# Kernel tuning notes

Hardware: AMD Instinct MI355X
Metric: run time of the kernel (lower is better)

The kernel has to match this reference:

```python
import jax, jax.numpy as jnp
import numpy as np

D, H, K, L, NB = 128, 8, 16, 16, 2
N, E, MN, ME = 100_000, 800_000, 1_000, 8_000
VOCAB, BT, VP = 50_000, 256, 15
_SQD, _SQK = float(np.sqrt(D)), float(np.sqrt(K))


def _segment_softmax(score, seg, num):
    m = jax.ops.segment_max(score, seg, num_segments=num)
    e = jnp.exp(score - m[seg])
    z = jax.ops.segment_sum(e, seg, num_segments=num)
    return e / (z[seg] + 1e-9)


def _meta_learner(feat, u, W2, W1):
    # latent-attention factorization: feat [n,D] -> 2d param [n,H,K], 1d param [n,H]
    w = jax.nn.softmax((feat @ u.T) / _SQD, axis=-1)  # [n,L]
    return jnp.einsum('nl,lhk->nhk', w, W2), w @ W1


def _conv(feat, src, dst, p2n, p1n, p2e, p1e, Wq, Wk, Wv, Wo):
    # HeteroAttnConv: multi-head attention message passing modulated by
    # per-node (p2n,p1n) and per-edge (p2e,p1e) meta parameters.
    n = feat.shape[0]
    q = (feat @ Wq).reshape(n, H, K) * p2n
    kf = (feat @ Wk).reshape(n, H, K)
    v = (feat @ Wv).reshape(n, H, K)
    ke = kf[src] * p2e                                   # [e,H,K]
    score = (q[dst] * ke).sum(-1) / _SQK + p1e + p1n[dst]  # [e,H]
    attn = _segment_softmax(score, dst, n)
    agg = jax.ops.segment_sum(attn[..., None] * v[src], dst, num_segments=n).reshape(n, D)
    return jax.nn.relu(agg @ Wo), ke.reshape(-1, D)


def _forward(emb, u, W2lat, W1lat, Wq_m, Wk_m, Wv_m, Wo_m, Wq, Wk, Wv, Wo,
             node_vals, meta_node_vals, src, dst, meta_src, meta_dst,
             meta_node_id, meta_edge_id, target_idx,
             static_vals, static_src, static_dst):
    # _init_meta_param: static param-name graph, copy_u/sum then meta_learner
    fs = emb[static_vals]
    agg = jax.ops.segment_sum(fs[static_src], static_dst, num_segments=VP)
    p2s, p1s = _meta_learner(agg, u, W2lat, W1lat)
    base_tw, base_n1, base_n2 = p1s[0], p1s[3], p2s[6]   # target_weight, node 1d, node 2d
    base_e1, base_e2 = p1s[9], p2s[12]                   # edge 1d, edge 2d

    meta_feat = emb[meta_node_vals]
    feat = emb[node_vals]
    # _asign_param_to_graph(meta_graph): broadcast base buffers only
    mp2n = jnp.broadcast_to(base_n2, (MN, H, K))
    mp1n = jnp.broadcast_to(base_n1, (MN, H))
    mp2e = jnp.broadcast_to(base_e2, (ME, H, K))
    mp1e = jnp.broadcast_to(base_e1, (ME, H))

    out = jnp.zeros((BT, 1), feat.dtype)
    for b in range(NB):
        pre_meta, pre = meta_feat, feat
        meta_feat, meta_edge_feat = _conv(meta_feat, meta_src, meta_dst,
                                          mp2n, mp1n, mp2e, mp1e,
                                          Wq_m[b], Wk_m[b], Wv_m[b], Wo_m[b])
        # _asign_param_to_graph(graph, meta_node_feat, meta_edge_feat):
        # base repeat + indexed add of meta_learner outputs
        p2mn, p1mn = _meta_learner(meta_feat, u, W2lat, W1lat)
        p2me, p1me = _meta_learner(meta_edge_feat, u, W2lat, W1lat)
        p2n = base_n2[None] + p2mn[meta_node_id]
        p1n = base_n1[None] + p1mn[meta_node_id]
        tw = base_tw[None] + p1mn[meta_node_id]
        p2e = base_e2[None] + p2me[meta_edge_id]
        p1e = base_e1[None] + p1me[meta_edge_id]
        feat, _ = _conv(feat, src, dst, p2n, p1n, p2e, p1e,
                        Wq[b], Wk[b], Wv[b], Wo[b])
        # block residual
        meta_feat = meta_feat + pre_meta
        feat = feat + pre
        # Target: per-target-node weighted readout with target_weight param
        logit = jnp.einsum('th,thk->t', tw[target_idx],
                           feat[target_idx].reshape(BT, H, K))
        out = out + logit[:, None]
    return out / NB


def setup_inputs() -> dict:
    key = jax.random.key(0)
    ks = jax.random.split(key, 24)
    s = 0.05
    inp = {}
    inp['emb'] = jax.random.normal(ks[0], (VOCAB, D), jnp.float32) * s
    inp['u'] = jax.random.normal(ks[1], (L, D), jnp.float32) * s
    inp['W2lat'] = jax.random.normal(ks[2], (L, H, K), jnp.float32) * s
    inp['W1lat'] = jax.random.normal(ks[3], (L, H), jnp.float32) * s
    for i, nm in enumerate(['Wq_m', 'Wk_m', 'Wv_m', 'Wo_m', 'Wq', 'Wk', 'Wv', 'Wo']):
        inp[nm] = jax.random.normal(ks[4 + i], (NB, D, D), jnp.float32) / np.sqrt(D)
    inp['node_vals'] = jax.random.randint(ks[12], (N,), 0, VOCAB)
    inp['meta_node_vals'] = jax.random.randint(ks[13], (MN,), 0, VOCAB)
    inp['src'] = jax.random.randint(ks[14], (E,), 0, N)
    inp['dst'] = jax.random.randint(ks[15], (E,), 0, N)
    inp['meta_src'] = jax.random.randint(ks[16], (ME,), 0, MN)
    inp['meta_dst'] = jax.random.randint(ks[17], (ME,), 0, MN)
    inp['meta_node_id'] = jax.random.randint(ks[18], (N,), 0, MN)
    inp['meta_edge_id'] = jax.random.randint(ks[19], (E,), 0, ME)
    inp['target_idx'] = jax.random.randint(ks[20], (BT,), 0, N)
    # static param-name graph: 5 names x (1 name node + 2 token nodes), tokens->name
    name_pos = np.arange(5) * 3
    inp['static_vals'] = jax.random.randint(ks[21], (VP,), 0, VOCAB)
    inp['static_src'] = jnp.asarray(np.stack([name_pos + 1, name_pos + 2], 1).reshape(-1), jnp.int32)
    inp['static_dst'] = jnp.asarray(np.repeat(name_pos, 2), jnp.int32)
    return inp


def reference(emb, u, W2lat, W1lat, Wq_m, Wk_m, Wv_m, Wo_m, Wq, Wk, Wv, Wo,
              node_vals, meta_node_vals, src, dst, meta_src, meta_dst,
              meta_node_id, meta_edge_id, target_idx,
              static_vals, static_src, static_dst):
    return _forward(emb, u, W2lat, W1lat, Wq_m, Wk_m, Wv_m, Wo_m, Wq, Wk, Wv, Wo,
                    node_vals, meta_node_vals, src, dst, meta_src, meta_dst,
                    meta_node_id, meta_edge_id, target_idx,
                    static_vals, static_src, static_dst)
```

## Files before the change

### kernel.cpp

```cpp
#include <hip/hip_runtime.h>
#include <hip/hip_bf16.h>
#include <hip/hip_fp8.h>

#define DD   128
#define HH   8

typedef short bf16x8 __attribute__((ext_vector_type(8)));
typedef float f32x4  __attribute__((ext_vector_type(4)));
typedef float f32x2  __attribute__((ext_vector_type(2)));

__device__ __forceinline__ float b2f(unsigned short v){
  union { unsigned int u; float f; } x; x.u = ((unsigned int)v) << 16; return x.f;
}
__device__ __forceinline__ unsigned short f2b(float f){
  __hip_bfloat16 h = __float2bfloat16(f);
  return *(unsigned short*)&h;
}
__device__ __forceinline__ unsigned char f2f8(float x){
  __hip_fp8_e4m3 h(x);
  return h.__x;
}
__device__ __forceinline__ float f82f(unsigned char b){
  __hip_fp8_e4m3 h; h.__x = b;
  return (float)h;
// ... 11 lines not shown
  o[2]=f82f((w>>16)&0xff); o[3]=f82f((w>>24)&0xff);
}
struct __align__(8) us4 { unsigned short x,y,z,w; };
struct __align__(16) us8 { unsigned short s[8]; };

__device__ __forceinline__ float gld(const void* p, size_t i, bool f32){
  if (f32) return ((const float*)p)[i];
  return b2f(((const unsigned short*)p)[i]);
}

__device__ __forceinline__ void gll16(const void* g, void* l){
  __builtin_amdgcn_global_load_lds(
      (const __attribute__((address_space(1))) unsigned int*)g,
      (__attribute__((address_space(3))) unsigned int*)l, 16, 0, 0);
}

struct WPtrs { const void* p[8]; };
__global__ __launch_bounds__(256) void w_repack16(
    WPtrs W, unsigned short* __restrict__ stage, int NBt,
    const int* __restrict__ dflag)
{
  const bool wf32 = (*dflag) != 0;
  int idx = blockIdx.x >> 6;
  int ti = idx / NBt, bi = idx - ti*NBt;
  size_t bo = (size_t)bi*DD*DD;
  int i = (blockIdx.x & 63)*256 + threadIdx.x;
  int k = i >> 7, n = i & 127;
  float x;
  if (wf32) x = ((const float*)W.p[ti])[bo + i];
  else      x = b2f(((const unsigned short*)W.p[ti])[bo + i]);
  stage[(size_t)idx*DD*DD + n*DD + k] = f2b(x);
}

enum { EPI_STORE=0, EPI_SCALE_CONST=1, EPI_SCALE_GATHER=2, EPI_RELU=3,
       EPI_RELU_RES=4, EPI_RELU_RES2=5 };

#define CPAD 132


template<int EPI, bool INB, bool OUTB>
__global__ __launch_bounds__(256) void gemm128m(
    const void* __restrict__ Av, const unsigned short* __restrict__ Bt,
    void* __restrict__ Cv, int M,
    const unsigned short* __restrict__ Rb,
    const float* __restrict__ Rf, float* __restrict__ C2)
{
  __shared__ __align__(16) unsigned short Asb[64*128];
  __shared__ __align__(16) unsigned short Btb[16896];
  const int tid = threadIdx.x;
  const int wave = tid >> 6, lane = tid & 63;
  const int row0 = blockIdx.x * 64;

  if (INB){
    const char* Ab = (const char*)Av;
    int n4 = lane >> 4, c = lane & 15;
#pragma unroll
    for (int op=0; op<4; op++){
      int rA = wave*16 + op*4;
      int n = rA + n4;
      int gr = row0 + n; if (gr >= M) gr = M - 1;
      gll16(Ab + (size_t)gr*256 + ((size_t)((c ^ (n & 7)) << 4)), &Asb[rA*128]);
    }
  } else {
    const float* Af = (const float*)Av;
    int r = tid >> 2, cb = (tid & 3) * 32, rx = (r & 7) << 3;
    int gr = row0 + r;
#pragma unroll
// ... 44 lines not shown
  }
  __syncthreads();

  {
    int r = tid >> 2, cb = (tid & 3) * 32;
    int gr = row0 + r;
    if (gr < M){
#pragma unroll
      for (int j=0;j<8;j++){
        int c = cb + j*4;
        float4 o = *(float4*)&Cls[r*CPAD + c];
        if (EPI == EPI_RELU_RES){
          us4 rb = *(const us4*)(Rb + (size_t)gr*DD + c);
          o.x=fmaxf(o.x,0.f)+b2f(rb.x); o.y=fmaxf(o.y,0.f)+b2f(rb.y);
          o.z=fmaxf(o.z,0.f)+b2f(rb.z); o.w=fmaxf(o.w,0.f)+b2f(rb.w);
        } else if (EPI == EPI_RELU_RES2){
          o.x=fmaxf(o.x,0.f); o.y=fmaxf(o.y,0.f); o.z=fmaxf(o.z,0.f); o.w=fmaxf(o.w,0.f);
          float4 rf = *(const float4*)(Rf + (size_t)gr*DD + c);
          *(float4*)(C2 + (size_t)gr*DD + c) =
              make_float4(o.x+rf.x, o.y+rf.y, o.z+rf.z, o.w+rf.w);
        }
        if (OUTB){
          us4 ob; ob.x=f2b(o.x); ob.y=f2b(o.y); ob.z=f2b(o.z); ob.w=f2b(o.w);
          *(us4*)((unsigned short*)Cv + (size_t)gr*DD + c) = ob;
        } else {
          *(float4*)((float*)Cv + (size_t)gr*DD + c) = o;
        }
      }
    }
  }
}

template<int EPIQ, bool INB, bool FP8KV>
__global__ __launch_bounds__(256) void gemm_qkv(
    const void* __restrict__ Av,
    const unsigned short* __restrict__ Btq, const unsigned short* __restrict__ Btk,
    const unsigned short* __restrict__ Btv,
    void* __restrict__ Cq, void* __restrict__ Ck, int stK,
    void* __restrict__ Cvo, int stV, int M,
    const float* __restrict__ svec, const float* __restrict__ P2,
    const int* __restrict__ gidx)
{
  __shared__ __align__(16) unsigned short Asb[64*128];
  __shared__ __align__(16) unsigned short Btb[16896];
  const int tid = threadIdx.x;
  const int wave = tid >> 6, lane = tid & 63;
  const int row0 = blockIdx.x * 64;

  if (INB){
    const char* Ab = (const char*)Av;
    int n4 = lane >> 4, c = lane & 15;
#pragma unroll
    for (int op=0; op<4; op++){
      int rA = wave*16 + op*4;
      int n = rA + n4;
      int gr = row0 + n; if (gr >= M) gr = M - 1;
      gll16(Ab + (size_t)gr*256 + ((size_t)((c ^ (n & 7)) << 4)), &Asb[rA*128]);
    }
  } else {
    const float* Af = (const float*)Av;
    int r = tid >> 2, cb = (tid & 3) * 32, rx = (r & 7) << 3;
    int gr = row0 + r;
#pragma unroll
    for (int j=0;j<8;j++){
      int cc = cb + j*4;
      float4 val = make_float4(0.f,0.f,0.f,0.f);
      if (gr < M) val = *(const float4*)(Af + (size_t)gr*DD + cc);
      us4 o; o.x=f2b(val.x); o.y=f2b(val.y); o.z=f2b(val.z); o.w=f2b(val.w);
      *(us4*)&Asb[r*128 + (cc ^ rx)] = o;
    }
  }

  const unsigned short* Bts[3] = {Btq, Btk, Btv};
  void* Cs[3] = {Cq, Ck, Cvo};
  const int sts[3] = {DD, stK, stV};
  const int am = (lane & 15), kq = (lane >> 4) * 8, axr = (am & 7) << 3;

  for (int ph=0; ph<3; ph++){
    {
      const unsigned short* Bt = Bts[ph];
// ... 10 lines not shown
    f32x4 acc[8];
#pragma unroll
    for (int t=0;t<8;t++) acc[t] = (f32x4){0.f,0.f,0.f,0.f};
#pragma unroll
    for (int k0=0;k0<128;k0+=32){
      int xo = (k0 + kq) ^ axr;
      bf16x8 a = *(bf16x8*)&Asb[(wave*16 + am)*128 + xo];
#pragma unroll
      for (int t=0;t<8;t++){
        bf16x8 b = *(bf16x8*)&Btb[(t*16 + am)*128 + xo];
        acc[t] = __builtin_amdgcn_mfma_f32_16x16x32_bf16(a, b, acc[t], 0,0,0);
      }
    }
    __syncthreads();
    float* Cls = (float*)Btb;
    {
      int rr = wave*16 + (lane>>4)*4;
      int cc = lane & 15;
#pragma unroll
      for (int t=0;t<8;t++)
#pragma unroll
        for (int r=0;r<4;r++)
          Cls[(rr + r)*CPAD + t*16 + cc] = acc[t][r];
    }
    __syncthreads();
    {
      int r = tid >> 2, cb = (tid & 3) * 32;
      int gr = row0 + r;
      if (gr < M){
#pragma unroll
        for (int j=0;j<8;j++){
          int c = cb + j*4;
          float4 o = *(float4*)&Cls[r*CPAD + c];
          if (ph == 0){
            if (EPIQ == EPI_SCALE_GATHER){
              int g = gidx[gr];
              const float* p = P2 + (size_t)g*DD + c;
              o.x*=(svec[c+0]+p[0]); o.y*=(svec[c+1]+p[1]);
              o.z*=(svec[c+2]+p[2]); o.w*=(svec[c+3]+p[3]);
            } else {
              o.x*=svec[c+0]; o.y*=svec[c+1]; o.z*=svec[c+2]; o.w*=svec[c+3];
            }
          }
          if (FP8KV && ph > 0){
            unsigned char* Cb = (unsigned char*)Cs[ph];
            uchar4 ob;
            ob.x=f2f8(o.x*8.f); ob.y=f2f8(o.y*8.f);
            ob.z=f2f8(o.z*8.f); ob.w=f2f8(o.w*8.f);
            *(uchar4*)(Cb + (size_t)gr*256 + c) = ob;
          } else {
            us4 ob; ob.x=f2b(o.x); ob.y=f2b(o.y); ob.z=f2b(o.z); ob.w=f2b(o.w);
            *(us4*)((unsigned short*)Cs[ph] + (size_t)gr*sts[ph] + c) = ob;
          }
        }
      }
    }
    __syncthreads();
  }
}

__global__ __launch_bounds__(256) void k_static(
    const void* __restrict__ emb, const int* __restrict__ svals,
    const int* __restrict__ ssrc, const int* __restrict__ sdst,
    const void* __restrict__ u, const void* __restrict__ W2,
    const void* __restrict__ W1, float* __restrict__ base, int nsrc,
    int* __restrict__ dflag)
{
  __shared__ float sagg[15][128];
  __shared__ float ssc[15][16];
  __shared__ float sww[15][16];
  __shared__ int swf;
  const int t = threadIdx.x;
  if (t < 64){
    float m = 0.f;
    for (int i=t; i<128; i+=64){
      float x = fabsf(b2f(((const unsigned short*)emb)[i]));
      if (x < 1e30f) m = fmaxf(m, x);
    }
#pragma unroll
    for (int s=1;s<64;s<<=1) m = fmaxf(m, __shfl_xor(m, s, 64));
    if (t==0){ int f = (m > 1e4f) ? 1 : 0; *dflag = f; swf = f; }
  }
  for (int i=t;i<15*128;i+=256) ((float*)sagg)[i]=0.f;
  __syncthreads();
  const bool wf32 = (swf != 0);
  if (t < 128){
    for (int i=0;i<nsrc;i++){
      int row = sdst[i]; int vr = svals[ssrc[i]];
      sagg[row][t] += gld(emb, (size_t)vr*DD + t, wf32);
    }
// ... 192 lines not shown
  if (d >= NM) return;
  int lane = threadIdx.x & 63;
  const float* be2 = base+152; const float* be1 = base+16; const float* bn1 = base+8;
  size_t dq = (size_t)d*DD;
  float q0 = b2f(qm[dq+lane]), q1 = b2f(qm[dq+64+lane]);
  float w0 = be2[lane], w1 = be2[64+lane];
  int h0 = lane>>4, h1 = h0+4;
  float bias0 = be1[h0] + bn1[h0];
  float bias1 = be1[h1] + bn1[h1];
  float z0=0.f, z1=0.f, a0=0.f, a1=0.f;
  int i0 = rowptr[d], i1 = rowptr[d+1];
  for (int i=i0; i<i1; i++){
    int s = esrc[i], e = eorig[i];
    size_t so=(size_t)s*DD, eo=(size_t)e*DD;
    float ke0 = b2f(kfm[so+lane])    * w0;
    float ke1 = b2f(kfm[so+64+lane]) * w1;
    mef[eo+lane]=f2b(ke0); mef[eo+64+lane]=f2b(ke1);
    float p0 = q0*ke0, p1 = q1*ke1;
#pragma unroll
    for (int m=1;m<16;m<<=1){ p0 += __shfl_xor(p0,m,64); p1 += __shfl_xor(p1,m,64); }
    float e0 = __expf(p0*0.25f + bias0);
    float e1 = __expf(p1*0.25f + bias1);
    z0 += e0; z1 += e1;
    a0 += e0*b2f(vm[so+lane]);
    a1 += e1*b2f(vm[so+64+lane]);
  }
  float inv0 = 1.f/(z0 + 1e-9f);
  float inv1 = 1.f/(z1 + 1e-9f);
  agg[dq+lane]    = a0*inv0;
  agg[dq+64+lane] = a1*inv1;
}

__global__ __launch_bounds__(128) void learner2(
    const float* __restrict__ Xa, const unsigned short* __restrict__ Xb, int Ma,
    const void* __restrict__ u, const void* __restrict__ W2,
    const void* __restrict__ W1,
    float* __restrict__ p2a, float* __restrict__ p1a,
    unsigned short* __restrict__ w2me, unsigned short* __restrict__ p1b,
    const float* __restrict__ base, const int* __restrict__ dflag)
{
  __shared__ float sX[128];
  __shared__ float st[16];
  __shared__ float sw[16];
  const bool wf32 = (*dflag) != 0;
  const int blk = blockIdx.x, t = threadIdx.x;
  const bool isB = (blk >= Ma);
  const int m = isB ? (blk - Ma) : blk;
  if (isB) sX[t] = b2f(Xb[(size_t)m*DD + t]);
  else     sX[t] = Xa[(size_t)m*DD + t];
  __syncthreads();
  int l = t>>3, j = t&7;
  float part = 0.f;
  for (int d=j*16; d<j*16+16; d++) part += sX[d]*gld(u, l*128+d, wf32);
  part += __shfl_xor(part,1,64); part += __shfl_xor(part,2,64); part += __shfl_xor(part,4,64);
  if (j==0) st[l] = part * 0.08838834764831845f;
  __syncthreads();
  float mx=-1e30f;
  for (int i=0;i<16;i++) mx = fmaxf(mx, st[i]);
  float ssum=0.f;
  for (int i=0;i<16;i++) ssum += __expf(st[i]-mx);
  float inv = 1.f/ssum;
  if (t<16) sw[t] = __expf(st[t]-mx)*inv;
  __syncthreads();
  float a=0.f;
  for (int i=0;i<16;i++) a += sw[i]*gld(W2, i*128+t, wf32);
  if (isB) w2me[(size_t)m*DD+t] = f2b(base[152+t] + a);
  else     p2a[(size_t)m*DD+t] = a;
  if (t<8){
    float bb=0.f;
    for (int i=0;i<16;i++) bb += sw[i]*gld(W1, i*8+t, wf32);
    if (isB) p1b[(size_t)m*HH+t] = f2b(bb);
    else     p1a[(size_t)m*HH+t] = bb;
  }
}

__global__ __launch_bounds__(256) void edge_fused(
    const int* __restrict__ rowptr, const int* __restrict__ epack,
    const int* __restrict__ mnid,
    const unsigned short* __restrict__ q, const unsigned char* __restrict__ kv8,
    const unsigned short* __restrict__ w2me, const unsigned short* __restrict__ p1me,
    const float* __restrict__ p1mn, const float* __restrict__ base,
    unsigned short* __restrict__ aggb, int N)
{
  int wv = blockIdx.x*4 + (threadIdx.x>>6);
  int lane = threadIdx.x & 63;
  int grp = lane >> 4, l16 = lane & 15;
  int d = wv*4 + grp;
  if (d >= N) return;
  int c8 = l16 * 8;
  int h = l16 >> 1;

  int i0 = rowptr[d], i1 = rowptr[d+1];
  float bias = base[16+h] + base[8+h] + p1mn[(size_t)mnid[d]*HH + h];
  size_t dq = (size_t)d*DD;
  float qv[8];
  {
    uint4 qraw = *(const uint4*)(q + dq + c8);
    const unsigned short* qh = (const unsigned short*)&qraw;
#pragma unroll
    for (int j=0;j<8;j++) qv[j] = b2f(qh[j])*0.03125f;
  }

  float zh = 0.f;
  float a[8];
#pragma unroll
  for (int j=0;j<8;j++) a[j] = 0.f;

  int i = i0;
  for (; i + 1 < i1; i += 2){
    unsigned int v0p = (unsigned int)epack[i];
    unsigned int v1p = (unsigned int)epack[i+1];
    int s0 = v0p & 0x1FFFF, me0 = v0p >> 17;
    int s1 = v1p & 0x1FFFF, me1 = v1p >> 17;
    size_t kvo0 = (size_t)s0*256, mo0 = (size_t)me0*DD;
    size_t kvo1 = (size_t)s1*256, mo1 = (size_t)me1*DD;
    uint2 kraw0 = *(const uint2*)(kv8 + kvo0 + c8);
    uint2 vraw0 = *(const uint2*)(kv8 + kvo0 + 128 + c8);
    uint4 wraw0 = *(const uint4*)(w2me + mo0 + c8);
    float pm0 = b2f(p1me[(size_t)me0*HH + h]);
    uint2 kraw1 = *(const uint2*)(kv8 + kvo1 + c8);
    uint2 vraw1 = *(const uint2*)(kv8 + kvo1 + 128 + c8);
    uint4 wraw1 = *(const uint4*)(w2me + mo1 + c8);
    float pm1 = b2f(p1me[(size_t)me1*HH + h]);
    float k0f[8], v0f[8], k1f[8], v1f[8];
    cvt4(kraw0.x, k0f); cvt4(kraw0.y, k0f+4);
    cvt4(vraw0.x, v0f); cvt4(vraw0.y, v0f+4);
    cvt4(kraw1.x, k1f); cvt4(kraw1.y, k1f+4);
    cvt4(vraw1.x, v1f); cvt4(vraw1.y, v1f+4);
    const unsigned short* wh0 = (const unsigned short*)&wraw0;
    const unsigned short* wh1 = (const unsigned short*)&wraw1;
    float pA = 0.f, pB = 0.f;
#pragma unroll
    for (int j=0;j<8;j++){
      pA += qv[j]*(k0f[j]*b2f(wh0[j]));
      pB += qv[j]*(k1f[j]*b2f(wh1[j]));
    }
    pA += __shfl_xor(pA, 1, 64);
    pB += __shfl_xor(pB, 1, 64);
    float ex0 = __expf(pA + bias + pm0);
    float ex1 = __expf(pB + bias + pm1);
    zh += ex0 + ex1;
#pragma unroll
    for (int j=0;j<8;j++) a[j] += ex0*v0f[j] + ex1*v1f[j];
  }
  if (i < i1){
    unsigned int vp = (unsigned int)epack[i];
    int s = vp & 0x1FFFF, me = vp >> 17;
    size_t kvo = (size_t)s*256, mo = (size_t)me*DD;
    uint2 kraw = *(const uint2*)(kv8 + kvo + c8);
    uint2 vraw = *(const uint2*)(kv8 + kvo + 128 + c8);
    uint4 wraw = *(const uint4*)(w2me + mo + c8);
    float pm = b2f(p1me[(size_t)me*HH + h]);
    float kf[8], vf[8];
    cvt4(kraw.x, kf); cvt4(kraw.y, kf+4);
    cvt4(vraw.x, vf); cvt4(vraw.y, vf+4);
    const unsigned short* wh = (const unsigned short*)&wraw;
    float p = 0.f;
#pragma unroll
    for (int j=0;j<8;j++) p += qv[j]*(kf[j]*b2f(wh[j]));
    p += __shfl_xor(p, 1, 64);
    float ex = __expf(p + bias + pm);
    zh += ex;
#pragma unroll
    for (int j=0;j<8;j++) a[j] += ex*vf[j];
  }

  float inv = 0.125f / (zh + 1e-9f);
  us8 o;
#pragma unroll
  for (int j=0;j<8;j++) o.s[j] = f2b(a[j]*inv);
  *(us8*)(aggb + dq + c8) = o;
}

__global__ __launch_bounds__(256) void readout(
    const int* __restrict__ tgt, const int* __restrict__ mnid,
    const unsigned short* __restrict__ featb, const float* __restrict__ p1mn,
    const float* __restrict__ base, float* __restrict__ acc,
    void* __restrict__ out, int last, float invNB, int BT,
    const int* __restrict__ dflag)
{
  int t = blockIdx.x*256 + threadIdx.x;
  int ti = t >> 4, l16 = t & 15;
  if (ti >= BT) return;
  int idx = tgt[ti]; int mn = mnid[idx];
  int h = l16 >> 1;
  float tw = base[h] + p1mn[(size_t)mn*HH + h];
  uint4 raw = *(const uint4*)(featb + (size_t)idx*DD + l16*8);
  const unsigned short* hw = (const unsigned short*)&raw;
  float s = 0.f;
#pragma unroll
  for (int j=0;j<8;j++) s += b2f(hw[j]);
  float part = tw * s;
  part += __shfl_xor(part, 1, 64);
  part += __shfl_xor(part, 2, 64);
  part += __shfl_xor(part, 4, 64);
  part += __shfl_xor(part, 8, 64);
  if (l16 == 0){
    if (!last) acc[ti] = part;
    else {
      float r = (acc[ti] + part) * invNB;
      if ((*dflag) != 0) ((float*)out)[ti] = r;
      else ((__hip_bfloat16*)out)[ti] = __float2bfloat16(r);
    }
  }
// ... 73 lines not shown

  k_static<<<1,256,0,stream>>>(emb, static_vals, static_src, static_dst,
                               u, W2lat, W1lat, base, NSRC, dflag);
  gather_rows2<<<((N+MN)*16+255)/256,256,0,stream>>>(emb, node_vals, feat, N,
      meta_node_vals, meta_feat, MN, dflag);

  const int nbE  = (E+255)/256, nbME = (ME+255)/256;
  const int nb3B = (N+255)/256, nb3M = (MN+255)/256;
  zeroi<<<(N+MN+255)/256,256,0,stream>>>(degAll, N+MN);
  k_hist2<<<nbE+nbME,256,0,stream>>>(dst, meta_dst, deg, deg_m, E, ME, nbE);
  k_scan1b<<<nb_scan+nb_scan_m,256,0,stream>>>(deg, rowptr, bsum, N, nb_scan,
      deg_m, rowptr_m, bsum_m, MN);
  k_scan3b<<<nb3B+nb3M,256,0,stream>>>(rowptr, bsum, cursor, N, nb3B, nb_scan,
      rowptr_m, bsum_m, cursor_m, MN, nb_scan_m);
  k_scatter2<<<nbE+nbME,256,0,stream>>>(dst, src, meta_edge_id, cursor,
      epack, E, nbE, meta_dst, meta_src, cursor_m, esrc_m, eorig_m, ME);

  w_repack16<<<8*NB*64,256,0,stream>>>(wptrs, wstage, NB, dflag);

  const int gm = (MN+63)/64;
  const int gN = (N+63)/64;
  const float invNB = 1.0f/(float)NB;

  for (int b=0;b<NB;b++){
    const unsigned short* wq_m = wstage + (size_t)(0*NB+b)*DD*DD;
    const unsigned short* wk_m = wstage + (size_t)(1*NB+b)*DD*DD;
    const unsigned short* wv_m = wstage + (size_t)(2*NB+b)*DD*DD;
    const unsigned short* wo_m = wstage + (size_t)(3*NB+b)*DD*DD;
    const unsigned short* wqb  = wstage + (size_t)(4*NB+b)*DD*DD;
    const unsigned short* wkb  = wstage + (size_t)(5*NB+b)*DD*DD;
    const unsigned short* wvb  = wstage + (size_t)(6*NB+b)*DD*DD;
    const unsigned short* wob  = wstage + (size_t)(7*NB+b)*DD*DD;

    gemm_qkv<EPI_SCALE_CONST,false,false><<<gm,256,0,stream>>>(meta_feat,
        wq_m, wk_m, wv_m, q_m, kf_m, DD, v_m, DD, MN, base_n2, nullptr, nullptr);
    edge_meta_csr<<<(MN+3)/4,256,0,stream>>>(rowptr_m, esrc_m, eorig_m,
        q_m, kf_m, v_m, base, mef, agg_m, MN);
    gemm128m<EPI_RELU_RES2,false,false><<<gm,256,0,stream>>>(agg_m, wo_m,
        meta_out, MN, nullptr, meta_feat, meta_feat);
    learner2<<<MN+ME,128,0,stream>>>(meta_out, mef, MN, u, W2lat, W1lat,
        p2mn, p1mn, w2me, p1me, base, dflag);

    gemm_qkv<EPI_SCALE_GATHER,true,true><<<gN,256,0,stream>>>(feat, wqb, wkb, wvb,
        q, kv8, 0, kv8 + 128, 0, N, base_n2, p2mn, meta_node_id);
    edge_fused<<<(N+15)/16,256,0,stream>>>(rowptr, epack,
        meta_node_id, q, kv8, w2me, p1me, p1mn, base, aggb, N);
    gemm128m<EPI_RELU_RES,true,true><<<gN,256,0,stream>>>(aggb, wob, feat, N,
        feat, nullptr, nullptr);

    readout<<<(BT*16+255)/256,256,0,stream>>>(target_idx, meta_node_id, feat, p1mn,
        base, acc, d_out, (b==NB-1) ? 1 : 0, invNB, BT, dflag);
  }
}
```

Baseline: 647.9 us.

## Merge big and meta QKV GEMMs, defer node q-scaling into edge kernel

The big-graph QKV projection no longer depends on the meta learner output. The per-node p2 scale is now applied to q inside the edge attention kernel, so the big and meta QKV GEMMs run as one launch before the meta stage. The edge kernel switches from 16 lanes per destination to 8 lanes per destination (one per head), which drops the cross-lane shuffle. learner2 caches u/W2/W1 in registers and handles four rows per block. The trade-offs are higher register pressure in the edge kernel and a q stored in bf16 before it is scaled.

```diff
diff --git a/kernel.cpp b/kernel.cpp
--- a/kernel.cpp
+++ b/kernel.cpp
@@ -67,7 +67,7 @@
   stage[(size_t)idx*DD*DD + n*DD + k] = f2b(x);
 }
 
-enum { EPI_STORE=0, EPI_SCALE_CONST=1, EPI_SCALE_GATHER=2, EPI_RELU=3,
+enum { EPI_STORE=0, EPI_SCALE_CONST=1, EPI_RELU=3,
        EPI_RELU_RES=4, EPI_RELU_RES2=5 };
 
 #define CPAD 132
@@ -178,20 +178,18 @@
 }
 
 template<int EPIQ, bool INB, bool FP8KV>
-__global__ __launch_bounds__(256) void gemm_qkv(
+__device__ __forceinline__ void qkv_body(
+    unsigned short* Asb, unsigned short* Btb, int blk,
     const void* __restrict__ Av,
     const unsigned short* __restrict__ Btq, const unsigned short* __restrict__ Btk,
     const unsigned short* __restrict__ Btv,
     void* __restrict__ Cq, void* __restrict__ Ck, int stK,
     void* __restrict__ Cvo, int stV, int M,
-    const float* __restrict__ svec, const float* __restrict__ P2,
-    const int* __restrict__ gidx)
+    const float* __restrict__ svec)
 {
-  __shared__ __align__(16) unsigned short Asb[64*128];
-  __shared__ __align__(16) unsigned short Btb[16896];
   const int tid = threadIdx.x;
   const int wave = tid >> 6, lane = tid & 63;
-  const int row0 = blockIdx.x * 64;
+  const int row0 = blk * 64;
 
   if (INB){
     const char* Ab = (const char*)Av;
@@ -268,15 +266,8 @@
         for (int j=0;j<8;j++){
           int c = cb + j*4;
           float4 o = *(float4*)&Cls[r*CPAD + c];
-          if (ph == 0){
-            if (EPIQ == EPI_SCALE_GATHER){
-              int g = gidx[gr];
-              const float* p = P2 + (size_t)g*DD + c;
-              o.x*=(svec[c+0]+p[0]); o.y*=(svec[c+1]+p[1]);
-              o.z*=(svec[c+2]+p[2]); o.w*=(svec[c+3]+p[3]);
-            } else {
-              o.x*=svec[c+0]; o.y*=svec[c+1]; o.z*=svec[c+2]; o.w*=svec[c+3];
-            }
+          if (ph == 0 && EPIQ == EPI_SCALE_CONST){
+            o.x*=svec[c+0]; o.y*=svec[c+1]; o.z*=svec[c+2]; o.w*=svec[c+3];
           }
           if (FP8KV && ph > 0){
             unsigned char* Cb = (unsigned char*)Cs[ph];
@@ -292,6 +283,28 @@
       }
     }
     __syncthreads();
+  }
+}
+
+__global__ __launch_bounds__(256) void gemm_qkv2(
+    const unsigned short* __restrict__ featB, const float* __restrict__ featM,
+    const unsigned short* __restrict__ wqb, const unsigned short* __restrict__ wkb,
+    const unsigned short* __restrict__ wvb,
+    const unsigned short* __restrict__ wqm, const unsigned short* __restrict__ wkm,
+    const unsigned short* __restrict__ wvm,
+    unsigned short* __restrict__ qB, unsigned char* __restrict__ kv8,
+    unsigned short* __restrict__ qM, unsigned short* __restrict__ kfM,
+    unsigned short* __restrict__ vM,
+    int Nbig, int Nmeta, int gN, const float* __restrict__ svec)
+{
+  __shared__ __align__(16) unsigned short Asb[64*128];
+  __shared__ __align__(16) unsigned short Btb[16896];
+  if (blockIdx.x < gN){
+    qkv_body<EPI_STORE,true,true>(Asb, Btb, blockIdx.x, featB,
+        wqb, wkb, wvb, qB, kv8, 0, kv8 + 128, 0, Nbig, svec);
+  } else {
+    qkv_body<EPI_SCALE_CONST,false,false>(Asb, Btb, blockIdx.x - gN, featM,
+        wqm, wkm, wvm, qM, kfM, DD, vM, DD, Nmeta, svec);
   }
 }
 
@@ -550,7 +563,8 @@
 }
 
 __global__ __launch_bounds__(128) void learner2(
-    const float* __restrict__ Xa, const unsigned short* __restrict__ Xb, int Ma,
+    const float* __restrict__ Xa, const unsigned short* __restrict__ Xb,
+    int Ma, int Mtot,
     const void* __restrict__ u, const void* __restrict__ W2,
     const void* __restrict__ W1,
     float* __restrict__ p2a, float* __restrict__ p1a,
@@ -561,34 +575,51 @@
   __shared__ float st[16];
   __shared__ float sw[16];
   const bool wf32 = (*dflag) != 0;
-  const int blk = blockIdx.x, t = threadIdx.x;
-  const bool isB = (blk >= Ma);
-  const int m = isB ? (blk - Ma) : blk;
-  if (isB) sX[t] = b2f(Xb[(size_t)m*DD + t]);
-  else     sX[t] = Xa[(size_t)m*DD + t];
-  __syncthreads();
-  int l = t>>3, j = t&7;
-  float part = 0.f;
-  for (int d=j*16; d<j*16+16; d++) part += sX[d]*gld(u, l*128+d, wf32);
-  part += __shfl_xor(part,1,64); part += __shfl_xor(part,2,64); part += __shfl_xor(part,4,64);
-  if (j==0) st[l] = part * 0.08838834764831845f;
-  __syncthreads();
-  float mx=-1e30f;
-  for (int i=0;i<16;i++) mx = fmaxf(mx, st[i]);
-  float ssum=0.f;
-  for (int i=0;i<16;i++) ssum += __expf(st[i]-mx);
-  float inv = 1.f/ssum;
-  if (t<16) sw[t] = __expf(st[t]-mx)*inv;
-  __syncthreads();
-  float a=0.f;
-  for (int i=0;i<16;i++) a += sw[i]*gld(W2, i*128+t, wf32);
-  if (isB) w2me[(size_t)m*DD+t] = f2b(base[152+t] + a);
-  else     p2a[(size_t)m*DD+t] = a;
-  if (t<8){
-    float bb=0.f;
-    for (int i=0;i<16;i++) bb += sw[i]*gld(W1, i*8+t, wf32);
-    if (isB) p1b[(size_t)m*HH+t] = f2b(bb);
-    else     p1a[(size_t)m*HH+t] = bb;
+  const int t = threadIdx.x;
+  const int l = t>>3, j = t&7;
+  float uc[16], w2c[16], w1c[16];
+#pragma unroll
+  for (int m=0;m<16;m++) uc[m] = gld(u, (size_t)l*128 + j*16 + m, wf32);
+#pragma unroll
+  for (int i=0;i<16;i++) w2c[i] = gld(W2, (size_t)i*128 + t, wf32);
+  if (t < 8){
+#pragma unroll
+    for (int i=0;i<16;i++) w1c[i] = gld(W1, (size_t)i*8 + t, wf32);
+  }
+  for (int rr=0; rr<4; rr++){
+    int row = blockIdx.x*4 + rr;
+    if (row >= Mtot) break;
+    const bool isB = (row >= Ma);
+    const int m = isB ? (row - Ma) : row;
+    if (isB) sX[t] = b2f(Xb[(size_t)m*DD + t]);
+    else     sX[t] = Xa[(size_t)m*DD + t];
+    __syncthreads();
+    float part = 0.f;
+#pragma unroll
+    for (int mm=0;mm<16;mm++) part += sX[j*16+mm]*uc[mm];
+    part += __shfl_xor(part,1,64); part += __shfl_xor(part,2,64); part += __shfl_xor(part,4,64);
+    if (j==0) st[l] = part * 0.08838834764831845f;
+    __syncthreads();
+    float mx=-1e30f;
+    for (int i=0;i<16;i++) mx = fmaxf(mx, st[i]);
+    float ssum=0.f;
+    for (int i=0;i<16;i++) ssum += __expf(st[i]-mx);
+    float inv = 1.f/ssum;
+    if (t<16) sw[t] = __expf(st[t]-mx)*inv;
+    __syncthreads();
+    float a=0.f;
+#pragma unroll
+    for (int i=0;i<16;i++) a += sw[i]*w2c[i];
+    if (isB) w2me[(size_t)m*DD+t] = f2b(base[152+t] + a);
+    else     p2a[(size_t)m*DD+t] = a;
+    if (t<8){
+      float bb=0.f;
+#pragma unroll
+      for (int i=0;i<16;i++) bb += sw[i]*w1c[i];
+      if (isB) p1b[(size_t)m*HH+t] = f2b(bb);
+      else     p1a[(size_t)m*HH+t] = bb;
+    }
+    __syncthreads();
   }
 }
 
@@ -597,32 +628,40 @@
     const int* __restrict__ mnid,
     const unsigned short* __restrict__ q, const unsigned char* __restrict__ kv8,
     const unsigned short* __restrict__ w2me, const unsigned short* __restrict__ p1me,
-    const float* __restrict__ p1mn, const float* __restrict__ base,
+    const float* __restrict__ p1mn, const float* __restrict__ p2mn,
+    const float* __restrict__ base,
     unsigned short* __restrict__ aggb, int N)
 {
-  int wv = blockIdx.x*4 + (threadIdx.x>>6);
-  int lane = threadIdx.x & 63;
-  int grp = lane >> 4, l16 = lane & 15;
-  int d = wv*4 + grp;
+  const int tid = threadIdx.x;
+  const int lane = tid & 63;
+  const int l8 = lane & 7;
+  const int d = blockIdx.x*32 + (tid>>6)*8 + (lane>>3);
   if (d >= N) return;
-  int c8 = l16 * 8;
-  int h = l16 >> 1;
-
-  int i0 = rowptr[d], i1 = rowptr[d+1];
-  float bias = base[16+h] + base[8+h] + p1mn[(size_t)mnid[d]*HH + h];
-  size_t dq = (size_t)d*DD;
-  float qv[8];
+  const int h = l8;
+  const int c16 = l8*16;
+  const int i0 = rowptr[d], i1 = rowptr[d+1];
+  const int mn = mnid[d];
+  const float bias = base[16+h] + base[8+h] + p1mn[(size_t)mn*HH + h];
+  const size_t dq = (size_t)d*DD;
+
+  float qv[16];
   {
-    uint4 qraw = *(const uint4*)(q + dq + c8);
-    const unsigned short* qh = (const unsigned short*)&qraw;
-#pragma unroll
-    for (int j=0;j<8;j++) qv[j] = b2f(qh[j])*0.03125f;
+    uint4 qr0 = *(const uint4*)(q + dq + c16);
+    uint4 qr1 = *(const uint4*)(q + dq + c16 + 8);
+    const unsigned short* qh0 = (const unsigned short*)&qr0;
+    const unsigned short* qh1 = (const unsigned short*)&qr1;
+    const float* p2 = p2mn + (size_t)mn*DD + c16;
+    const float* sv = base + 24 + c16;
+#pragma unroll
+    for (int j=0;j<8;j++) qv[j]   = b2f(qh0[j]) * (sv[j]   + p2[j])   * 0.03125f;
+#pragma unroll
+    for (int j=0;j<8;j++) qv[8+j] = b2f(qh1[j]) * (sv[8+j] + p2[8+j]) * 0.03125f;
   }
 
   float zh = 0.f;
-  float a[8];
-#pragma unroll
-  for (int j=0;j<8;j++) a[j] = 0.f;
+  float a[16];
+#pragma unroll
+  for (int j=0;j<16;j++) a[j] = 0.f;
 
   int i = i0;
   for (; i + 1 < i1; i += 2){
@@ -630,64 +669,79 @@
     unsigned int v1p = (unsigned int)epack[i+1];
     int s0 = v0p & 0x1FFFF, me0 = v0p >> 17;
     int s1 = v1p & 0x1FFFF, me1 = v1p >> 17;
-    size_t kvo0 = (size_t)s0*256, mo0 = (size_t)me0*DD;
-    size_t kvo1 = (size_t)s1*256, mo1 = (size_t)me1*DD;
-    uint2 kraw0 = *(const uint2*)(kv8 + kvo0 + c8);
-    uint2 vraw0 = *(const uint2*)(kv8 + kvo0 + 128 + c8);
-    uint4 wraw0 = *(const uint4*)(w2me + mo0 + c8);
+    const unsigned char* kv0 = kv8 + (size_t)s0*256 + c16;
+    const unsigned char* kv1 = kv8 + (size_t)s1*256 + c16;
+    const unsigned short* w0 = w2me + (size_t)me0*DD + c16;
+    const unsigned short* w1 = w2me + (size_t)me1*DD + c16;
+    uint4 kraw0 = *(const uint4*)kv0;
+    uint4 vraw0 = *(const uint4*)(kv0 + 128);
+    us8 w0a = *(const us8*)w0;
+    us8 w0b = *(const us8*)(w0 + 8);
     float pm0 = b2f(p1me[(size_t)me0*HH + h]);
-    uint2 kraw1 = *(const uint2*)(kv8 + kvo1 + c8);
-    uint2 vraw1 = *(const uint2*)(kv8 + kvo1 + 128 + c8);
-    uint4 wraw1 = *(const uint4*)(w2me + mo1 + c8);
+    uint4 kraw1 = *(const uint4*)kv1;
+    uint4 vraw1 = *(const uint4*)(kv1 + 128);
+    us8 w1a = *(const us8*)w1;
+    us8 w1b = *(const us8*)(w1 + 8);
     float pm1 = b2f(p1me[(size_t)me1*HH + h]);
-    float k0f[8], v0f[8], k1f[8], v1f[8];
-    cvt4(kraw0.x, k0f); cvt4(kraw0.y, k0f+4);
-    cvt4(vraw0.x, v0f); cvt4(vraw0.y, v0f+4);
-    cvt4(kraw1.x, k1f); cvt4(kraw1.y, k1f+4);
-    cvt4(vraw1.x, v1f); cvt4(vraw1.y, v1f+4);
-    const unsigned short* wh0 = (const unsigned short*)&wraw0;
-    const unsigned short* wh1 = (const unsigned short*)&wraw1;
+
+    float k0f[16], k1f[16];
+    cvt4(kraw0.x,k0f);   cvt4(kraw0.y,k0f+4);
+    cvt4(kraw0.z,k0f+8); cvt4(kraw0.w,k0f+12);
+    cvt4(kraw1.x,k1f);   cvt4(kraw1.y,k1f+4);
+    cvt4(kraw1.z,k1f+8); cvt4(kraw1.w,k1f+12);
     float pA = 0.f, pB = 0.f;
 #pragma unroll
     for (int j=0;j<8;j++){
-      pA += qv[j]*(k0f[j]*b2f(wh0[j]));
-      pB += qv[j]*(k1f[j]*b2f(wh1[j]));
-    }
-    pA += __shfl_xor(pA, 1, 64);
-    pB += __shfl_xor(pB, 1, 64);
+      pA += qv[j]  *(k0f[j]  *b2f(w0a.s[j]));
+      pA += qv[8+j]*(k0f[8+j]*b2f(w0b.s[j]));
+      pB += qv[j]  *(k1f[j]  *b2f(w1a.s[j]));
+      pB += qv[8+j]*(k1f[8+j]*b2f(w1b.s[j]));
+    }
     float ex0 = __expf(pA + bias + pm0);
     float ex1 = __expf(pB + bias + pm1);
     zh += ex0 + ex1;
-#pragma unroll
-    for (int j=0;j<8;j++) a[j] += ex0*v0f[j] + ex1*v1f[j];
+    float v0f[16], v1f[16];
+    cvt4(vraw0.x,v0f);   cvt4(vraw0.y,v0f+4);
+    cvt4(vraw0.z,v0f+8); cvt4(vraw0.w,v0f+12);
+    cvt4(vraw1.x,v1f);   cvt4(vraw1.y,v1f+4);
+    cvt4(vraw1.z,v1f+8); cvt4(vraw1.w,v1f+12);
+#pragma unroll
+    for (int j=0;j<16;j++) a[j] += ex0*v0f[j] + ex1*v1f[j];
   }
   if (i < i1){
     unsigned int vp = (unsigned int)epack[i];
     int s = vp & 0x1FFFF, me = vp >> 17;
-    size_t kvo = (size_t)s*256, mo = (size_t)me*DD;
-    uint2 kraw = *(const uint2*)(kv8 + kvo + c8);
-    uint2 vraw = *(const uint2*)(kv8 + kvo + 128 + c8);
-    uint4 wraw = *(const uint4*)(w2me + mo + c8);
+    const unsigned char* kv0 = kv8 + (size_t)s*256 + c16;
+    const unsigned short* w0 = w2me + (size_t)me*DD + c16;
+    uint4 kraw = *(const uint4*)kv0;
+    uint4 vraw = *(const uint4*)(kv0 + 128);
+    us8 wa = *(const us8*)w0;
+    us8 wb = *(const us8*)(w0 + 8);
     float pm = b2f(p1me[(size_t)me*HH + h]);
-    float kf[8], vf[8];
-    cvt4(kraw.x, kf); cvt4(kraw.y, kf+4);
-    cvt4(vraw.x, vf); cvt4(vraw.y, vf+4);
-    const unsigned short* wh = (const unsigned short*)&wraw;
+    float kf[16];
+    cvt4(kraw.x,kf);   cvt4(kraw.y,kf+4);
+    cvt4(kraw.z,kf+8); cvt4(kraw.w,kf+12);
     float p = 0.f;
 #pragma unroll
-    for (int j=0;j<8;j++) p += qv[j]*(kf[j]*b2f(wh[j]));
-    p += __shfl_xor(p, 1, 64);
+    for (int j=0;j<8;j++){
+      p += qv[j]  *(kf[j]  *b2f(wa.s[j]));
+      p += qv[8+j]*(kf[8+j]*b2f(wb.s[j]));
+    }
     float ex = __expf(p + bias + pm);
     zh += ex;
-#pragma unroll
-    for (int j=0;j<8;j++) a[j] += ex*vf[j];
+    float vf[16];
+    cvt4(vraw.x,vf);   cvt4(vraw.y,vf+4);
+    cvt4(vraw.z,vf+8); cvt4(vraw.w,vf+12);
+#pragma unroll
+    for (int j=0;j<16;j++) a[j] += ex*vf[j];
   }
 
   float inv = 0.125f / (zh + 1e-9f);
-  us8 o;
-#pragma unroll
-  for (int j=0;j<8;j++) o.s[j] = f2b(a[j]*inv);
-  *(us8*)(aggb + dq + c8) = o;
+  us8 o0, o1;
+#pragma unroll
+  for (int j=0;j<8;j++){ o0.s[j] = f2b(a[j]*inv); o1.s[j] = f2b(a[8+j]*inv); }
+  *(us8*)(aggb + dq + c16)     = o0;
+  *(us8*)(aggb + dq + c16 + 8) = o1;
 }
 
 __global__ __launch_bounds__(256) void readout(
@@ -827,19 +881,19 @@
     const unsigned short* wvb  = wstage + (size_t)(6*NB+b)*DD*DD;
     const unsigned short* wob  = wstage + (size_t)(7*NB+b)*DD*DD;
 
-    gemm_qkv<EPI_SCALE_CONST,false,false><<<gm,256,0,stream>>>(meta_feat,
-        wq_m, wk_m, wv_m, q_m, kf_m, DD, v_m, DD, MN, base_n2, nullptr, nullptr);
+    gemm_qkv2<<<gN+gm,256,0,stream>>>(feat, meta_feat,
+        wqb, wkb, wvb, wq_m, wk_m, wv_m,
+        q, kv8, q_m, kf_m, v_m, N, MN, gN, base_n2);
+
     edge_meta_csr<<<(MN+3)/4,256,0,stream>>>(rowptr_m, esrc_m, eorig_m,
         q_m, kf_m, v_m, base, mef, agg_m, MN);
     gemm128m<EPI_RELU_RES2,false,false><<<gm,256,0,stream>>>(agg_m, wo_m,
         meta_out, MN, nullptr, meta_feat, meta_feat);
-    learner2<<<MN+ME,128,0,stream>>>(meta_out, mef, MN, u, W2lat, W1lat,
-        p2mn, p1mn, w2me, p1me, base, dflag);
-
-    gemm_qkv<EPI_SCALE_GATHER,true,true><<<gN,256,0,stream>>>(feat, wqb, wkb, wvb,
-        q, kv8, 0, kv8 + 128, 0, N, base_n2, p2mn, meta_node_id);
-    edge_fused<<<(N+15)/16,256,0,stream>>>(rowptr, epack,
-        meta_node_id, q, kv8, w2me, p1me, p1mn, base, aggb, N);
+    learner2<<<(MN+ME+3)/4,128,0,stream>>>(meta_out, mef, MN, MN+ME,
+        u, W2lat, W1lat, p2mn, p1mn, w2me, p1me, base, dflag);
+
+    edge_fused<<<(N+31)/32,256,0,stream>>>(rowptr, epack,
+        meta_node_id, q, kv8, w2me, p1me, p1mn, p2mn, base, aggb, N);
     gemm128m<EPI_RELU_RES,true,true><<<gN,256,0,stream>>>(aggb, wob, feat, N,
         feat, nullptr, nullptr);
 
```

Measured after the change: 573.9 us. 11.4% less time.

## Merge big and meta QKV GEMMs, defer q scaling to edge kernel, batch learner rows

Applied to the files above, without the earlier changes.

The big-graph QKV GEMM no longer needs the per-meta-node q scale, so that scale moves into the edge attention kernel. This lets it run in the same launch as the meta-graph QKV GEMM, ahead of the meta conv chain, which cuts one launch and removes a dependency. learner2 now handles four rows per block and keeps u/W2/W1 in registers instead of reloading them for every row. The edge loop is unrolled by four to keep more gathers in flight, at the cost of extra register pressure and per-edge scale work in edge_fused.

```diff
diff --git a/kernel.cpp b/kernel.cpp
--- a/kernel.cpp
+++ b/kernel.cpp
@@ -67,7 +67,7 @@
   stage[(size_t)idx*DD*DD + n*DD + k] = f2b(x);
 }
 
-enum { EPI_STORE=0, EPI_SCALE_CONST=1, EPI_SCALE_GATHER=2, EPI_RELU=3,
+enum { EPI_STORE=0, EPI_SCALE_CONST=1, EPI_RELU=3,
        EPI_RELU_RES=4, EPI_RELU_RES2=5 };
 
 #define CPAD 132
@@ -178,20 +178,18 @@
 }
 
 template<int EPIQ, bool INB, bool FP8KV>
-__global__ __launch_bounds__(256) void gemm_qkv(
+__device__ __forceinline__ void qkv_body(
+    unsigned short* Asb, unsigned short* Btb, int blk,
     const void* __restrict__ Av,
     const unsigned short* __restrict__ Btq, const unsigned short* __restrict__ Btk,
     const unsigned short* __restrict__ Btv,
     void* __restrict__ Cq, void* __restrict__ Ck, int stK,
     void* __restrict__ Cvo, int stV, int M,
-    const float* __restrict__ svec, const float* __restrict__ P2,
-    const int* __restrict__ gidx)
+    const float* __restrict__ svec)
 {
-  __shared__ __align__(16) unsigned short Asb[64*128];
-  __shared__ __align__(16) unsigned short Btb[16896];
   const int tid = threadIdx.x;
   const int wave = tid >> 6, lane = tid & 63;
-  const int row0 = blockIdx.x * 64;
+  const int row0 = blk * 64;
 
   if (INB){
     const char* Ab = (const char*)Av;
@@ -268,15 +266,8 @@
         for (int j=0;j<8;j++){
           int c = cb + j*4;
           float4 o = *(float4*)&Cls[r*CPAD + c];
-          if (ph == 0){
-            if (EPIQ == EPI_SCALE_GATHER){
-              int g = gidx[gr];
-              const float* p = P2 + (size_t)g*DD + c;
-              o.x*=(svec[c+0]+p[0]); o.y*=(svec[c+1]+p[1]);
-              o.z*=(svec[c+2]+p[2]); o.w*=(svec[c+3]+p[3]);
-            } else {
-              o.x*=svec[c+0]; o.y*=svec[c+1]; o.z*=svec[c+2]; o.w*=svec[c+3];
-            }
+          if (ph == 0 && EPIQ == EPI_SCALE_CONST){
+            o.x*=svec[c+0]; o.y*=svec[c+1]; o.z*=svec[c+2]; o.w*=svec[c+3];
           }
           if (FP8KV && ph > 0){
             unsigned char* Cb = (unsigned char*)Cs[ph];
@@ -292,6 +283,28 @@
       }
     }
     __syncthreads();
+  }
+}
+
+__global__ __launch_bounds__(256) void gemm_qkv2(
+    const unsigned short* __restrict__ featB, const float* __restrict__ featM,
+    const unsigned short* __restrict__ wqb, const unsigned short* __restrict__ wkb,
+    const unsigned short* __restrict__ wvb,
+    const unsigned short* __restrict__ wqm, const unsigned short* __restrict__ wkm,
+    const unsigned short* __restrict__ wvm,
+    unsigned short* __restrict__ qB, unsigned char* __restrict__ kv8,
+    unsigned short* __restrict__ qM, unsigned short* __restrict__ kfM,
+    unsigned short* __restrict__ vM,
+    int Nbig, int Nmeta, int gN, const float* __restrict__ svec)
+{
+  __shared__ __align__(16) unsigned short Asb[64*128];
+  __shared__ __align__(16) unsigned short Btb[16896];
+  if (blockIdx.x < gN){
+    qkv_body<EPI_STORE,true,true>(Asb, Btb, blockIdx.x, featB,
+        wqb, wkb, wvb, qB, kv8, 0, kv8 + 128, 0, Nbig, svec);
+  } else {
+    qkv_body<EPI_SCALE_CONST,false,false>(Asb, Btb, blockIdx.x - gN, featM,
+        wqm, wkm, wvm, qM, kfM, DD, vM, DD, Nmeta, svec);
   }
 }
 
@@ -550,7 +563,8 @@
 }
 
 __global__ __launch_bounds__(128) void learner2(
-    const float* __restrict__ Xa, const unsigned short* __restrict__ Xb, int Ma,
+    const float* __restrict__ Xa, const unsigned short* __restrict__ Xb,
+    int Ma, int Mtot,
     const void* __restrict__ u, const void* __restrict__ W2,
     const void* __restrict__ W1,
     float* __restrict__ p2a, float* __restrict__ p1a,
@@ -561,34 +575,51 @@
   __shared__ float st[16];
   __shared__ float sw[16];
   const bool wf32 = (*dflag) != 0;
-  const int blk = blockIdx.x, t = threadIdx.x;
-  const bool isB = (blk >= Ma);
-  const int m = isB ? (blk - Ma) : blk;
-  if (isB) sX[t] = b2f(Xb[(size_t)m*DD + t]);
-  else     sX[t] = Xa[(size_t)m*DD + t];
-  __syncthreads();
-  int l = t>>3, j = t&7;
-  float part = 0.f;
-  for (int d=j*16; d<j*16+16; d++) part += sX[d]*gld(u, l*128+d, wf32);
-  part += __shfl_xor(part,1,64); part += __shfl_xor(part,2,64); part += __shfl_xor(part,4,64);
-  if (j==0) st[l] = part * 0.08838834764831845f;
-  __syncthreads();
-  float mx=-1e30f;
-  for (int i=0;i<16;i++) mx = fmaxf(mx, st[i]);
-  float ssum=0.f;
-  for (int i=0;i<16;i++) ssum += __expf(st[i]-mx);
-  float inv = 1.f/ssum;
-  if (t<16) sw[t] = __expf(st[t]-mx)*inv;
-  __syncthreads();
-  float a=0.f;
-  for (int i=0;i<16;i++) a += sw[i]*gld(W2, i*128+t, wf32);
-  if (isB) w2me[(size_t)m*DD+t] = f2b(base[152+t] + a);
-  else     p2a[(size_t)m*DD+t] = a;
-  if (t<8){
-    float bb=0.f;
-    for (int i=0;i<16;i++) bb += sw[i]*gld(W1, i*8+t, wf32);
-    if (isB) p1b[(size_t)m*HH+t] = f2b(bb);
-    else     p1a[(size_t)m*HH+t] = bb;
+  const int t = threadIdx.x;
+  const int l = t>>3, j = t&7;
+  float uc[16], w2c[16], w1c[16];
+#pragma unroll
+  for (int m=0;m<16;m++) uc[m] = gld(u, (size_t)l*128 + j*16 + m, wf32);
+#pragma unroll
+  for (int i=0;i<16;i++) w2c[i] = gld(W2, (size_t)i*128 + t, wf32);
+  if (t < 8){
+#pragma unroll
+    for (int i=0;i<16;i++) w1c[i] = gld(W1, (size_t)i*8 + t, wf32);
+  }
+  for (int rr=0; rr<4; rr++){
+    int row = blockIdx.x*4 + rr;
+    if (row >= Mtot) break;
+    const bool isB = (row >= Ma);
+    const int m = isB ? (row - Ma) : row;
+    if (isB) sX[t] = b2f(Xb[(size_t)m*DD + t]);
+    else     sX[t] = Xa[(size_t)m*DD + t];
+    __syncthreads();
+    float part = 0.f;
+#pragma unroll
+    for (int mm=0;mm<16;mm++) part += sX[j*16+mm]*uc[mm];
+    part += __shfl_xor(part,1,64); part += __shfl_xor(part,2,64); part += __shfl_xor(part,4,64);
+    if (j==0) st[l] = part * 0.08838834764831845f;
+    __syncthreads();
+    float mx=-1e30f;
+    for (int i=0;i<16;i++) mx = fmaxf(mx, st[i]);
+    float ssum=0.f;
+    for (int i=0;i<16;i++) ssum += __expf(st[i]-mx);
+    float inv = 1.f/ssum;
+    if (t<16) sw[t] = __expf(st[t]-mx)*inv;
+    __syncthreads();
+    float a=0.f;
+#pragma unroll
+    for (int i=0;i<16;i++) a += sw[i]*w2c[i];
+    if (isB) w2me[(size_t)m*DD+t] = f2b(base[152+t] + a);
+    else     p2a[(size_t)m*DD+t] = a;
+    if (t<8){
+      float bb=0.f;
+#pragma unroll
+      for (int i=0;i<16;i++) bb += sw[i]*w1c[i];
+      if (isB) p1b[(size_t)m*HH+t] = f2b(bb);
+      else     p1a[(size_t)m*HH+t] = bb;
+    }
+    __syncthreads();
   }
 }
 
@@ -597,7 +628,8 @@
     const int* __restrict__ mnid,
     const unsigned short* __restrict__ q, const unsigned char* __restrict__ kv8,
     const unsigned short* __restrict__ w2me, const unsigned short* __restrict__ p1me,
-    const float* __restrict__ p1mn, const float* __restrict__ base,
+    const float* __restrict__ p1mn, const float* __restrict__ p2mn,
+    const float* __restrict__ base,
     unsigned short* __restrict__ aggb, int N)
 {
   int wv = blockIdx.x*4 + (threadIdx.x>>6);
@@ -609,14 +641,17 @@
   int h = l16 >> 1;
 
   int i0 = rowptr[d], i1 = rowptr[d+1];
-  float bias = base[16+h] + base[8+h] + p1mn[(size_t)mnid[d]*HH + h];
+  int mn = mnid[d];
+  float bias = base[16+h] + base[8+h] + p1mn[(size_t)mn*HH + h];
   size_t dq = (size_t)d*DD;
   float qv[8];
   {
     uint4 qraw = *(const uint4*)(q + dq + c8);
     const unsigned short* qh = (const unsigned short*)&qraw;
-#pragma unroll
-    for (int j=0;j<8;j++) qv[j] = b2f(qh[j])*0.03125f;
+    const float* p2 = p2mn + (size_t)mn*DD + c8;
+    const float* sv = base + 24 + c8;
+#pragma unroll
+    for (int j=0;j<8;j++) qv[j] = b2f(qh[j]) * (sv[j] + p2[j]) * 0.03125f;
   }
 
   float zh = 0.f;
@@ -625,20 +660,48 @@
   for (int j=0;j<8;j++) a[j] = 0.f;
 
   int i = i0;
+  for (; i + 3 < i1; i += 4){
+    uint2 kr[4], vr[4]; uint4 wr[4]; float pm[4];
+#pragma unroll
+    for (int t=0;t<4;t++){
+      unsigned int vp = (unsigned int)epack[i+t];
+      int s = vp & 0x1FFFF, me = vp >> 17;
+      const unsigned char* kv = kv8 + (size_t)s*256 + c8;
+      kr[t] = *(const uint2*)kv;
+      vr[t] = *(const uint2*)(kv + 128);
+      wr[t] = *(const uint4*)(w2me + (size_t)me*DD + c8);
+      pm[t] = b2f(p1me[(size_t)me*HH + h]);
+    }
+#pragma unroll
+    for (int t=0;t<4;t++){
+      float kf[8], vf[8];
+      cvt4(kr[t].x, kf); cvt4(kr[t].y, kf+4);
+      cvt4(vr[t].x, vf); cvt4(vr[t].y, vf+4);
+      const unsigned short* wh = (const unsigned short*)&wr[t];
+      float p = 0.f;
+#pragma unroll
+      for (int j=0;j<8;j++) p += qv[j]*(kf[j]*b2f(wh[j]));
+      p += __shfl_xor(p, 1, 64);
+      float ex = __expf(p + bias + pm[t]);
+      zh += ex;
+#pragma unroll
+      for (int j=0;j<8;j++) a[j] += ex*vf[j];
+    }
+  }
   for (; i + 1 < i1; i += 2){
     unsigned int v0p = (unsigned int)epack[i];
     unsigned int v1p = (unsigned int)epack[i+1];
     int s0 = v0p & 0x1FFFF, me0 = v0p >> 17;
     int s1 = v1p & 0x1FFFF, me1 = v1p >> 17;
-    size_t kvo0 = (size_t)s0*256, mo0 = (size_t)me0*DD;
-    size_t kvo1 = (size_t)s1*256, mo1 = (size_t)me1*DD;
-    uint2 kraw0 = *(const uint2*)(kv8 + kvo0 + c8);
-    uint2 vraw0 = *(const uint2*)(kv8 + kvo0 + 128 + c8);
-    uint4 wraw0 = *(const uint4*)(w2me + mo0 + c8);
+    const unsigned char* kv0 = kv8 + (size_t)s0*256 + c8;
+    const unsigned char* kv1 = kv8 + (size_t)s1*256 + c8;
+    uint2 kraw0 = *(const uint2*)kv0;
+    uint2 vraw0 = *(const uint2*)(kv0 + 128);
+    uint4 wraw0 = *(const uint4*)(w2me + (size_t)me0*DD + c8);
     float pm0 = b2f(p1me[(size_t)me0*HH + h]);
-    uint2 kraw1 = *(const uint2*)(kv8 + kvo1 + c8);
-    uint2 vraw1 = *(const uint2*)(kv8 + kvo1 + 128 + c8);
-    uint4 wraw1 = *(const uint4*)(w2me + mo1 + c8);
+    uint2 kraw1 = *(const uint2*)kv1;
+    uint2 vraw1 = *(const uint2*)(kv1 + 128);
+    uint4 wraw1 = *(const uint4*)(w2me + (size_t)me1*DD + c8);
     float pm1 = b2f(p1me[(size_t)me1*HH + h]);
     float k0f[8], v0f[8], k1f[8], v1f[8];
     cvt4(kraw0.x, k0f); cvt4(kraw0.y, k0f+4);
@@ -664,10 +727,10 @@
   if (i < i1){
     unsigned int vp = (unsigned int)epack[i];
     int s = vp & 0x1FFFF, me = vp >> 17;
-    size_t kvo = (size_t)s*256, mo = (size_t)me*DD;
-    uint2 kraw = *(const uint2*)(kv8 + kvo + c8);
-    uint2 vraw = *(const uint2*)(kv8 + kvo + 128 + c8);
-    uint4 wraw = *(const uint4*)(w2me + mo + c8);
+    const unsigned char* kv = kv8 + (size_t)s*256 + c8;
+    uint2 kraw = *(const uint2*)kv;
+    uint2 vraw = *(const uint2*)(kv + 128);
+    uint4 wraw = *(const uint4*)(w2me + (size_t)me*DD + c8);
     float pm = b2f(p1me[(size_t)me*HH + h]);
     float kf[8], vf[8];
     cvt4(kraw.x, kf); cvt4(kraw.y, kf+4);
@@ -827,19 +890,19 @@
     const unsigned short* wvb  = wstage + (size_t)(6*NB+b)*DD*DD;
     const unsigned short* wob  = wstage + (size_t)(7*NB+b)*DD*DD;
 
-    gemm_qkv<EPI_SCALE_CONST,false,false><<<gm,256,0,stream>>>(meta_feat,
-        wq_m, wk_m, wv_m, q_m, kf_m, DD, v_m, DD, MN, base_n2, nullptr, nullptr);
+    gemm_qkv2<<<gN+gm,256,0,stream>>>(feat, meta_feat,
+        wqb, wkb, wvb, wq_m, wk_m, wv_m,
+        q, kv8, q_m, kf_m, v_m, N, MN, gN, base_n2);
+
     edge_meta_csr<<<(MN+3)/4,256,0,stream>>>(rowptr_m, esrc_m, eorig_m,
         q_m, kf_m, v_m, base, mef, agg_m, MN);
     gemm128m<EPI_RELU_RES2,false,false><<<gm,256,0,stream>>>(agg_m, wo_m,
         meta_out, MN, nullptr, meta_feat, meta_feat);
-    learner2<<<MN+ME,128,0,stream>>>(meta_out, mef, MN, u, W2lat, W1lat,
-        p2mn, p1mn, w2me, p1me, base, dflag);
-
-    gemm_qkv<EPI_SCALE_GATHER,true,true><<<gN,256,0,stream>>>(feat, wqb, wkb, wvb,
-        q, kv8, 0, kv8 + 128, 0, N, base_n2, p2mn, meta_node_id);
+    learner2<<<(MN+ME+3)/4,128,0,stream>>>(meta_out, mef, MN, MN+ME,
+        u, W2lat, W1lat, p2mn, p1mn, w2me, p1me, base, dflag);
+
     edge_fused<<<(N+15)/16,256,0,stream>>>(rowptr, epack,
-        meta_node_id, q, kv8, w2me, p1me, p1mn, base, aggb, N);
+        meta_node_id, q, kv8, w2me, p1me, p1mn, p2mn, base, aggb, N);
     gemm128m<EPI_RELU_RES,true,true><<<gN,256,0,stream>>>(aggb, wob, feat, N,
         feat, nullptr, nullptr);
 
```

Result: faster. 571.9 us (-11.7%).
